# Kernel tuning notes

Hardware: AMD Instinct MI355X
Metric: run time of the kernel (lower is better)

## Reference

```python
import jax, jax.numpy as jnp
import numpy as np

N_NODES = 50000
N_EDGES = 800000
IN_DIM, HID_DIM, OUT_DIM = 256, 128, 64


def gcn_conv(x, edge_index, W, b):
    """PyG GCNConv: out = D^{-1/2} (A + I) D^{-1/2} (x @ W) + b."""
    n = x.shape[0]
    loops = jnp.arange(n, dtype=edge_index.dtype)
    src = jnp.concatenate([edge_index[0], loops])  # message source j
    dst = jnp.concatenate([edge_index[1], loops])  # aggregation target i
    ones = jnp.ones(src.shape[0], dtype=x.dtype)
    deg = jax.ops.segment_sum(ones, dst, num_segments=n)  # >= 1 (self-loops)
    dinv = jax.lax.rsqrt(deg)
    norm = dinv[src] * dinv[dst]                    # [E+N]
    h = x @ W                                       # [N, out] GEMM first (PyG order)
    msg = h[src] * norm[:, None]                    # gather + scale
    out = jax.ops.segment_sum(msg, dst, num_segments=n)  # scatter-add
    return out + b


def setup_inputs() -> dict:
    key = jax.random.key(0)
    k1, k2, k3, k4, k5 = jax.random.split(key, 5)
    x = jax.random.normal(k1, (N_NODES, IN_DIM), dtype=jnp.float32)
    edge_index = jax.random.randint(k2, (2, N_EDGES), 0, N_NODES, dtype=jnp.int64)
    # Glorot-ish init for weights, zero bias (PyG defaults)
    W1 = jax.random.normal(k3, (IN_DIM, HID_DIM), dtype=jnp.float32) / np.sqrt(IN_DIM)
    b1 = jnp.zeros((HID_DIM,), dtype=jnp.float32)
    W2 = jax.random.normal(k4, (HID_DIM, OUT_DIM), dtype=jnp.float32) / np.sqrt(HID_DIM)
    b2 = jnp.zeros((OUT_DIM,), dtype=jnp.float32)
    return {"x": x, "edge_index": edge_index, "W1": W1, "b1": b1, "W2": W2, "b2": b2}


def reference(x, edge_index, W1, b1, W2, b2):
    h = jax.nn.relu(gcn_conv(x, edge_index, W1, b1))
    return gcn_conv(h, edge_index, W2, b2)
```

## Files before the change

kernel.cpp:

```cpp
#include <hip/hip_runtime.h>

#define N_NODES 50000
#define N_EDGES 800000
#define IN_DIM 256
#define HID_DIM 128
#define OUT_DIM 64
#define CAP 64
#define HALF_E 400000

typedef __bf16 bf16x8 __attribute__((ext_vector_type(8)));
typedef float f32x4 __attribute__((ext_vector_type(4)));
typedef unsigned short u16x8 __attribute__((ext_vector_type(8)));
typedef unsigned short ushort_t;
typedef unsigned int uint_t;

__device__ __forceinline__ ushort_t f2bf(float f) {
    uint_t u = __float_as_uint(f);
    return (ushort_t)((u + 0x7fffu + ((u >> 16) & 1u)) >> 16);
}
__device__ __forceinline__ float bf_lo(uint_t u) { return __uint_as_float(u << 16); }
__device__ __forceinline__ float bf_hi(uint_t u) { return __uint_as_float(u & 0xffff0000u); }

__global__ __launch_bounds__(256) void k_init(const float* __restrict__ W1,
                                              ushort_t* __restrict__ w1t,
                                              const float* __restrict__ W2,
                                              ushort_t* __restrict__ w2t) {
    const int bid = blockIdx.x;
    const int t = threadIdx.x;
    if (bid < 128) {
        int id = bid * 256 + t;
        int k = id >> 7, c = id & 127;
        w1t[c * IN_DIM + k] = f2bf(W1[id]);
    } else {
        int id = (bid - 128) * 256 + t;
        int k = id >> 6, c = id & 63;
        w2t[c * HID_DIM + k] = f2bf(W2[id]);
    }
}

__global__ __launch_bounds__(256) void k_bucket(const int* __restrict__ srcs,
                                                const int* __restrict__ dsts,
                                                int* __restrict__ cur,
                                                ushort_t* __restrict__ es) {
    int t = blockIdx.x * 256 + threadIdx.x;
    if (t < HALF_E) {
        int d0 = dsts[t];
        int s0 = srcs[t];
        int d1 = dsts[t + HALF_E];
        int s1 = srcs[t + HALF_E];
        int p0 = atomicAdd(&cur[d0 << 4], 1);
        int p1 = atomicAdd(&cur[d1 << 4], 1);
        if (p0 < CAP) es[d0 * CAP + p0] = (ushort_t)s0;
        if (p1 < CAP) es[d1 * CAP + p1] = (ushort_t)s1;
    }
}

__global__ __launch_bounds__(64) void k_gemm1(const float* __restrict__ x,
                                              const ushort_t* __restrict__ w1t,
                                              const int* __restrict__ cur,
                                              float* __restrict__ dinv,
                                              int* __restrict__ ndeg,
                                              ushort_t* __restrict__ hb) {
    const int lane = threadIdx.x;
    const int l15 = lane & 15, quad = lane >> 4;
    if (lane < 16) {
        int i = blockIdx.x * 16 + lane;
        int deg = cur[i << 4];
        dinv[i] = rsqrtf((float)(deg + 1));
        ndeg[i] = min(deg, CAP);
    }
    const int row = blockIdx.x * 16 + l15;
    f32x4 acc[8];
#pragma unroll
    for (int n = 0; n < 8; ++n) acc[n] = (f32x4){0.f, 0.f, 0.f, 0.f};
    const float* xrow = x + (size_t)row * IN_DIM + quad * 8;
    const ushort_t* wbase = w1t + quad * 8;
#pragma unroll
    for (int t = 0; t < 8; ++t) {
        const float4* xp = (const float4*)(xrow + t * 32);
        float4 f0 = xp[0], f1 = xp[1];
        u16x8 au;
        au[0] = f2bf(f0.x); au[1] = f2bf(f0.y); au[2] = f2bf(f0.z); au[3] = f2bf(f0.w);
        au[4] = f2bf(f1.x); au[5] = f2bf(f1.y); au[6] = f2bf(f1.z); au[7] = f2bf(f1.w);
        bf16x8 a = __builtin_bit_cast(bf16x8, au);
#pragma unroll
        for (int n = 0; n < 8; ++n) {
            bf16x8 b = *(const bf16x8*)(wbase + (n * 16 + l15) * IN_DIM + t * 32);
            acc[n] = __builtin_amdgcn_mfma_f32_16x16x32_bf16(a, b, acc[n], 0, 0, 0);
        }
    }
    ushort_t* hrow = hb + ((size_t)blockIdx.x * 16 + quad * 4) * HID_DIM + l15;
#pragma unroll
    for (int n = 0; n < 8; ++n)
#pragma unroll
        for (int r = 0; r < 4; ++r)
            hrow[(size_t)r * HID_DIM + n * 16] = f2bf(acc[n][r]);
}

__global__ __launch_bounds__(256) void k_agg1(const ushort_t* __restrict__ hb,
                                              const int* __restrict__ ndeg,
                                              const float* __restrict__ dinv,
                                              const ushort_t* __restrict__ es,
                                              const float* __restrict__ b,
                                              ushort_t* __restrict__ hrelu) {
    const int i = blockIdx.x * 4 + (threadIdx.x >> 6);
    const int lane = threadIdx.x & 63;
    const float dv = dinv[i];
    const int n = ndeg[i];
    int   sj = 0;
    float nmj = 0.f;
    if (lane < n) {
        sj = (int)es[i * CAP + lane];
        nmj = dinv[sj] * dv;
    }
    uint_t u = *(const uint_t*)(hb + (size_t)i * HID_DIM + 2 * lane);
    float a0 = bf_lo(u) * dv * dv;
    float a1 = bf_hi(u) * dv * dv;
    int j = 0;
    for (; j + 8 <= n; j += 8) {
        int s0 = __shfl(sj, j),     s1 = __shfl(sj, j + 1);
        int s2 = __shfl(sj, j + 2), s3 = __shfl(sj, j + 3);
        int s4 = __shfl(sj, j + 4), s5 = __shfl(sj, j + 5);
        int s6 = __shfl(sj, j + 6), s7 = __shfl(sj, j + 7);
        float m0 = __shfl(nmj, j),     m1 = __shfl(nmj, j + 1);
        float m2 = __shfl(nmj, j + 2), m3 = __shfl(nmj, j + 3);
        float m4 = __shfl(nmj, j + 4), m5 = __shfl(nmj, j + 5);
        float m6 = __shfl(nmj, j + 6), m7 = __shfl(nmj, j + 7);
        uint_t v0 = *(const uint_t*)(hb + (size_t)s0 * HID_DIM + 2 * lane);
        uint_t v1 = *(const uint_t*)(hb + (size_t)s1 * HID_DIM + 2 * lane);
        uint_t v2 = *(const uint_t*)(hb + (size_t)s2 * HID_DIM + 2 * lane);
        uint_t v3 = *(const uint_t*)(hb + (size_t)s3 * HID_DIM + 2 * lane);
        uint_t v4 = *(const uint_t*)(hb + (size_t)s4 * HID_DIM + 2 * lane);
        uint_t v5 = *(const uint_t*)(hb + (size_t)s5 * HID_DIM + 2 * lane);
        uint_t v6 = *(const uint_t*)(hb + (size_t)s6 * HID_DIM + 2 * lane);
        uint_t v7 = *(const uint_t*)(hb + (size_t)s7 * HID_DIM + 2 * lane);
        a0 += bf_lo(v0) * m0 + bf_lo(v1) * m1 + bf_lo(v2) * m2 + bf_lo(v3) * m3
            + bf_lo(v4) * m4 + bf_lo(v5) * m5 + bf_lo(v6) * m6 + bf_lo(v7) * m7;
        a1 += bf_hi(v0) * m0 + bf_hi(v1) * m1 + bf_hi(v2) * m2 + bf_hi(v3) * m3
            + bf_hi(v4) * m4 + bf_hi(v5) * m5 + bf_hi(v6) * m6 + bf_hi(v7) * m7;
    }
    for (; j + 4 <= n; j += 4) {
        int s0 = __shfl(sj, j),     s1 = __shfl(sj, j + 1);
        int s2 = __shfl(sj, j + 2), s3 = __shfl(sj, j + 3);
        float m0 = __shfl(nmj, j),     m1 = __shfl(nmj, j + 1);
        float m2 = __shfl(nmj, j + 2), m3 = __shfl(nmj, j + 3);
        uint_t v0 = *(const uint_t*)(hb + (size_t)s0 * HID_DIM + 2 * lane);
        uint_t v1 = *(const uint_t*)(hb + (size_t)s1 * HID_DIM + 2 * lane);
        uint_t v2 = *(const uint_t*)(hb + (size_t)s2 * HID_DIM + 2 * lane);
        uint_t v3 = *(const uint_t*)(hb + (size_t)s3 * HID_DIM + 2 * lane);
        a0 += bf_lo(v0) * m0 + bf_lo(v1) * m1 + bf_lo(v2) * m2 + bf_lo(v3) * m3;
        a1 += bf_hi(v0) * m0 + bf_hi(v1) * m1 + bf_hi(v2) * m2 + bf_hi(v3) * m3;
    }
    for (; j < n; ++j) {
        int s = __shfl(sj, j);
        float nm = __shfl(nmj, j);
        uint_t v = *(const uint_t*)(hb + (size_t)s * HID_DIM + 2 * lane);
        a0 += bf_lo(v) * nm;
        a1 += bf_hi(v) * nm;
    }
    float v0 = a0 + b[2 * lane];     v0 = v0 > 0.f ? v0 : 0.f;
    float v1 = a1 + b[2 * lane + 1]; v1 = v1 > 0.f ? v1 : 0.f;
    *(uint_t*)(hrelu + (size_t)i * HID_DIM + 2 * lane) = ((uint_t)f2bf(v1) << 16) | f2bf(v0);
}

__global__ __launch_bounds__(64) void k_gemm2(const ushort_t* __restrict__ hrelu,
                                              const ushort_t* __restrict__ w2t,
                                              ushort_t* __restrict__ h2) {
    const int lane = threadIdx.x;
    const int l15 = lane & 15, quad = lane >> 4;
    const int row = blockIdx.x * 16 + l15;
    f32x4 acc[4];
#pragma unroll
    for (int n = 0; n < 4; ++n) acc[n] = (f32x4){0.f, 0.f, 0.f, 0.f};
    const ushort_t* arow = hrelu + (size_t)row * HID_DIM + quad * 8;
    const ushort_t* wbase = w2t + quad * 8;
#pragma unroll
    for (int t = 0; t < 4; ++t) {
        bf16x8 a = *(const bf16x8*)(arow + t * 32);
#pragma unroll
        for (int n = 0; n < 4; ++n) {
            bf16x8 b = *(const bf16x8*)(wbase + (n * 16 + l15) * HID_DIM + t * 32);
            acc[n] = __builtin_amdgcn_mfma_f32_16x16x32_bf16(a, b, acc[n], 0, 0, 0);
        }
    }
    ushort_t* orow = h2 + ((size_t)blockIdx.x * 16 + quad * 4) * OUT_DIM + l15;
#pragma unroll
    for (int n = 0; n < 4; ++n)
#pragma unroll
        for (int r = 0; r < 4; ++r)
            orow[(size_t)r * OUT_DIM + n * 16] = f2bf(acc[n][r]);
}

__global__ __launch_bounds__(256) void k_agg2(const ushort_t* __restrict__ h2,
                                              const int* __restrict__ ndeg,
                                              const float* __restrict__ dinv,
                                              const ushort_t* __restrict__ es,
                                              const float* __restrict__ b,
                                              float* __restrict__ out) {
    const int i = blockIdx.x * 4 + (threadIdx.x >> 6);
    const int lane = threadIdx.x & 63;
    const float dv = dinv[i];
    const int n = ndeg[i];
    int   sj = 0;
    float nmj = 0.f;
    if (lane < n) {
        sj = (int)es[i * CAP + lane];
        nmj = dinv[sj] * dv;
    }
    float acc = __uint_as_float(((uint_t)h2[(size_t)i * OUT_DIM + lane]) << 16) * dv * dv;
    int j = 0;
    for (; j + 8 <= n; j += 8) {
        int s0 = __shfl(sj, j),     s1 = __shfl(sj, j + 1);
        int s2 = __shfl(sj, j + 2), s3 = __shfl(sj, j + 3);
        int s4 = __shfl(sj, j + 4), s5 = __shfl(sj, j + 5);
        int s6 = __shfl(sj, j + 6), s7 = __shfl(sj, j + 7);
        float m0 = __shfl(nmj, j),     m1 = __shfl(nmj, j + 1);
        float m2 = __shfl(nmj, j + 2), m3 = __shfl(nmj, j + 3);
        float m4 = __shfl(nmj, j + 4), m5 = __shfl(nmj, j + 5);
        float m6 = __shfl(nmj, j + 6), m7 = __shfl(nmj, j + 7);
        float v0 = __uint_as_float(((uint_t)h2[(size_t)s0 * OUT_DIM + lane]) << 16);
        float v1 = __uint_as_float(((uint_t)h2[(size_t)s1 * OUT_DIM + lane]) << 16);
        float v2 = __uint_as_float(((uint_t)h2[(size_t)s2 * OUT_DIM + lane]) << 16);
        float v3 = __uint_as_float(((uint_t)h2[(size_t)s3 * OUT_DIM + lane]) << 16);
        float v4 = __uint_as_float(((uint_t)h2[(size_t)s4 * OUT_DIM + lane]) << 16);
        float v5 = __uint_as_float(((uint_t)h2[(size_t)s5 * OUT_DIM + lane]) << 16);
        float v6 = __uint_as_float(((uint_t)h2[(size_t)s6 * OUT_DIM + lane]) << 16);
        float v7 = __uint_as_float(((uint_t)h2[(size_t)s7 * OUT_DIM + lane]) << 16);
        acc += v0 * m0 + v1 * m1 + v2 * m2 + v3 * m3 + v4 * m4 + v5 * m5 + v6 * m6 + v7 * m7;
    }
    for (; j + 4 <= n; j += 4) {
        int s0 = __shfl(sj, j),     s1 = __shfl(sj, j + 1);
        int s2 = __shfl(sj, j + 2), s3 = __shfl(sj, j + 3);
        float m0 = __shfl(nmj, j),     m1 = __shfl(nmj, j + 1);
        float m2 = __shfl(nmj, j + 2), m3 = __shfl(nmj, j + 3);
        float v0 = __uint_as_float(((uint_t)h2[(size_t)s0 * OUT_DIM + lane]) << 16);
        float v1 = __uint_as_float(((uint_t)h2[(size_t)s1 * OUT_DIM + lane]) << 16);
        float v2 = __uint_as_float(((uint_t)h2[(size_t)s2 * OUT_DIM + lane]) << 16);
        float v3 = __uint_as_float(((uint_t)h2[(size_t)s3 * OUT_DIM + lane]) << 16);
        acc += v0 * m0 + v1 * m1 + v2 * m2 + v3 * m3;
    }
    for (; j < n; ++j) {
        int s = __shfl(sj, j);
        float nm = __shfl(nmj, j);
        acc += __uint_as_float(((uint_t)h2[(size_t)s * OUT_DIM + lane]) << 16) * nm;
    }
    out[(size_t)i * OUT_DIM + lane] = acc + b[lane];
}

extern "C" void kernel_launch(void* const* d_in, const int* in_sizes, int n_in,
                              void* d_out, int out_size, void* d_ws, size_t ws_size,
                              hipStream_t stream) {
    const float* x   = (const float*)d_in[0];
    const int*   ei  = (const int*)d_in[1];
    const float* W1  = (const float*)d_in[2];
    const float* b1  = (const float*)d_in[3];
    const float* W2  = (const float*)d_in[4];
    const float* b2  = (const float*)d_in[5];
    float* out = (float*)d_out;

    const int* srcs = ei;
    const int* dsts = ei + N_EDGES;

    char* ws = (char*)d_ws;
    size_t o = 0;
    auto alloc = [&](size_t bytes) { void* p = ws + o; o = (o + bytes + 511) & ~size_t(511); return p; };
    int*      cur   = (int*)     alloc((size_t)N_NODES * 16 * 4);
    float*    dinv  = (float*)   alloc(N_NODES * 4);
    int*      ndeg  = (int*)     alloc(N_NODES * 4);
    ushort_t* es    = (ushort_t*)alloc((size_t)N_NODES * CAP * 2);
    ushort_t* w1t   = (ushort_t*)alloc((size_t)IN_DIM * HID_DIM * 2);
    ushort_t* w2t   = (ushort_t*)alloc((size_t)HID_DIM * OUT_DIM * 2);
    ushort_t* hb    = (ushort_t*)alloc((size_t)N_NODES * HID_DIM * 2);
    ushort_t* hrelu = (ushort_t*)alloc((size_t)N_NODES * HID_DIM * 2);
    ushort_t* h2    = (ushort_t*)alloc((size_t)N_NODES * OUT_DIM * 2);

    hipMemsetAsync(cur, 0, (size_t)N_NODES * 16 * 4, stream);
    k_init  <<<160, 256, 0, stream>>>(W1, w1t, W2, w2t);
    k_bucket<<<1563, 256, 0, stream>>>(srcs, dsts, cur, es);
    k_gemm1 <<<N_NODES / 16, 64, 0, stream>>>(x, w1t, cur, dinv, ndeg, hb);
    k_agg1  <<<N_NODES / 4, 256, 0, stream>>>(hb, ndeg, dinv, es, b1, hrelu);
    k_gemm2 <<<N_NODES / 16, 64, 0, stream>>>(hrelu, w2t, h2);
    k_agg2  <<<N_NODES / 4, 256, 0, stream>>>(h2, ndeg, dinv, es, b2, out);
}
```

Before: 242.6 us.

## Replace global-atomic edge bucketing with two-pass LDS binning and fill

```diff
diff --git a/kernel.cpp b/kernel.cpp
--- a/kernel.cpp
+++ b/kernel.cpp
@@ -6,7 +6,12 @@
 #define HID_DIM 128
 #define OUT_DIM 64
 #define CAP 64
-#define HALF_E 400000
+
+#define K_BINS 256
+#define NPB 196
+#define BINCAP 4096
+#define CHUNK 4096
+#define N_BINWG 196
 
 typedef __bf16 bf16x8 __attribute__((ext_vector_type(8)));
 typedef float f32x4 __attribute__((ext_vector_type(4)));
@@ -38,37 +43,77 @@
     }
 }
 
-__global__ __launch_bounds__(256) void k_bucket(const int* __restrict__ srcs,
-                                                const int* __restrict__ dsts,
-                                                int* __restrict__ cur,
-                                                ushort_t* __restrict__ es) {
-    int t = blockIdx.x * 256 + threadIdx.x;
-    if (t < HALF_E) {
-        int d0 = dsts[t];
-        int s0 = srcs[t];
-        int d1 = dsts[t + HALF_E];
-        int s1 = srcs[t + HALF_E];
-        int p0 = atomicAdd(&cur[d0 << 4], 1);
-        int p1 = atomicAdd(&cur[d1 << 4], 1);
-        if (p0 < CAP) es[d0 * CAP + p0] = (ushort_t)s0;
-        if (p1 < CAP) es[d1 * CAP + p1] = (ushort_t)s1;
+__global__ __launch_bounds__(256) void k_bin(const int* __restrict__ srcs,
+                                             const int* __restrict__ dsts,
+                                             int* __restrict__ bin_cur,
+                                             uint_t* __restrict__ binbuf) {
+    __shared__ int lcnt[K_BINS];
+    __shared__ int lbase[K_BINS];
+    const int t = threadIdx.x;
+    lcnt[t] = 0;
+    __syncthreads();
+    const int start = blockIdx.x * CHUNK;
+    int b_[16]; int p_[16]; uint_t rec_[16];
+#pragma unroll
+    for (int k = 0; k < 16; ++k) {
+        int e = start + t + k * 256;
+        bool ok = (e < N_EDGES);
+        int d = ok ? dsts[e] : 0;
+        int s = ok ? srcs[e] : 0;
+        int b = d / NPB;
+        b_[k] = ok ? b : -1;
+        p_[k] = ok ? atomicAdd(&lcnt[b], 1) : 0;
+        rec_[k] = (uint_t)s | ((uint_t)(d - b * NPB) << 16);
+    }
+    __syncthreads();
+    lbase[t] = atomicAdd(&bin_cur[t], lcnt[t]);
+    __syncthreads();
+#pragma unroll
+    for (int k = 0; k < 16; ++k) {
+        if (b_[k] >= 0) {
+            int pos = lbase[b_[k]] + p_[k];
+            if (pos < BINCAP) binbuf[(size_t)b_[k] * BINCAP + pos] = rec_[k];
+        }
+    }
+}
+
+__global__ __launch_bounds__(256) void k_fill(const int* __restrict__ bin_cur,
+                                              const uint_t* __restrict__ binbuf,
+                                              ushort_t* __restrict__ es,
+                                              float* __restrict__ dinv,
+                                              int* __restrict__ ndeg) {
+    __shared__ int cnt[NPB];
+    __shared__ __align__(16) ushort_t pay[NPB][CAP];
+    const int b = blockIdx.x, t = threadIdx.x;
+    if (t < NPB) cnt[t] = 0;
+    __syncthreads();
+    const int n = min(bin_cur[b], BINCAP);
+    const uint_t* rec = binbuf + (size_t)b * BINCAP;
+    for (int e = t; e < n; e += 256) {
+        uint_t r = rec[e];
+        int dl = r >> 16;
+        int p = atomicAdd(&cnt[dl], 1);
+        if (p < CAP) pay[dl][p] = (ushort_t)(r & 0xffffu);
+    }
+    __syncthreads();
+    uint4* gdst = (uint4*)(es + (size_t)b * NPB * CAP);
+    const uint4* lsrc = (const uint4*)&pay[0][0];
+    for (int i = t; i < NPB * CAP / 8; i += 256) gdst[i] = lsrc[i];
+    if (t < NPB) {
+        int node = b * NPB + t;
+        if (node < N_NODES) {
+            int deg = cnt[t];
+            dinv[node] = rsqrtf((float)(deg + 1));
+            ndeg[node] = min(deg, CAP);
+        }
     }
 }
 
 __global__ __launch_bounds__(64) void k_gemm1(const float* __restrict__ x,
                                               const ushort_t* __restrict__ w1t,
-                                              const int* __restrict__ cur,
-                                              float* __restrict__ dinv,
-                                              int* __restrict__ ndeg,
                                               ushort_t* __restrict__ hb) {
     const int lane = threadIdx.x;
     const int l15 = lane & 15, quad = lane >> 4;
-    if (lane < 16) {
-        int i = blockIdx.x * 16 + lane;
-        int deg = cur[i << 4];
-        dinv[i] = rsqrtf((float)(deg + 1));
-        ndeg[i] = min(deg, CAP);
-    }
     const int row = blockIdx.x * 16 + l15;
     f32x4 acc[8];
 #pragma unroll
@@ -264,20 +309,22 @@
     char* ws = (char*)d_ws;
     size_t o = 0;
     auto alloc = [&](size_t bytes) { void* p = ws + o; o = (o + bytes + 511) & ~size_t(511); return p; };
-    int*      cur   = (int*)     alloc((size_t)N_NODES * 16 * 4);
+    int*      bin_cur = (int*)   alloc(K_BINS * 4);
     float*    dinv  = (float*)   alloc(N_NODES * 4);
     int*      ndeg  = (int*)     alloc(N_NODES * 4);
-    ushort_t* es    = (ushort_t*)alloc((size_t)N_NODES * CAP * 2);
+    ushort_t* es    = (ushort_t*)alloc((size_t)K_BINS * NPB * CAP * 2);
+    uint_t*   binbuf= (uint_t*)  alloc((size_t)K_BINS * BINCAP * 4);
     ushort_t* w1t   = (ushort_t*)alloc((size_t)IN_DIM * HID_DIM * 2);
     ushort_t* w2t   = (ushort_t*)alloc((size_t)HID_DIM * OUT_DIM * 2);
     ushort_t* hb    = (ushort_t*)alloc((size_t)N_NODES * HID_DIM * 2);
     ushort_t* hrelu = (ushort_t*)alloc((size_t)N_NODES * HID_DIM * 2);
     ushort_t* h2    = (ushort_t*)alloc((size_t)N_NODES * OUT_DIM * 2);
 
-    hipMemsetAsync(cur, 0, (size_t)N_NODES * 16 * 4, stream);
+    hipMemsetAsync(bin_cur, 0, K_BINS * 4, stream);
     k_init  <<<160, 256, 0, stream>>>(W1, w1t, W2, w2t);
-    k_bucket<<<1563, 256, 0, stream>>>(srcs, dsts, cur, es);
-    k_gemm1 <<<N_NODES / 16, 64, 0, stream>>>(x, w1t, cur, dinv, ndeg, hb);
+    k_bin   <<<N_BINWG, 256, 0, stream>>>(srcs, dsts, bin_cur, binbuf);
+    k_fill  <<<K_BINS, 256, 0, stream>>>(bin_cur, binbuf, es, dinv, ndeg);
+    k_gemm1 <<<N_NODES / 16, 64, 0, stream>>>(x, w1t, hb);
     k_agg1  <<<N_NODES / 4, 256, 0, stream>>>(hb, ndeg, dinv, es, b1, hrelu);
     k_gemm2 <<<N_NODES / 16, 64, 0, stream>>>(hrelu, w2t, h2);
     k_agg2  <<<N_NODES / 4, 256, 0, stream>>>(h2, ndeg, dinv, es, b2, out);
```

New measurement: 214.6 us. -11.6%, faster.
